# Kernel tuning notes

Hardware: AMD Instinct MI355X
Metric: run time of the kernel (lower is better)

The kernel has to match this reference:

```python
import jax, jax.numpy as jnp
import numpy as np

D_MODEL = 1024
N_HEAD = 16
HEAD_SIZE = D_MODEL // N_HEAD
SEQ = 2048
BATCH = 4
LN_EPS = 1e-5


def layer_norm(x, gamma, beta):
    mu = jnp.mean(x, axis=-1, keepdims=True)
    var = jnp.var(x, axis=-1, keepdims=True)
    return (x - mu) * jax.lax.rsqrt(var + LN_EPS) * gamma + beta


def setup_inputs() -> dict:
    key = jax.random.key(0)
    ks = jax.random.split(key, 12)
    s = 0.02
    return {
        "x": jax.random.normal(ks[0], (BATCH, SEQ, D_MODEL), jnp.float32),
        "Wq": jax.random.normal(ks[1], (N_HEAD, D_MODEL, HEAD_SIZE), jnp.float32) * s,
        "Wk": jax.random.normal(ks[2], (N_HEAD, D_MODEL, HEAD_SIZE), jnp.float32) * s,
        "Wv": jax.random.normal(ks[3], (N_HEAD, D_MODEL, HEAD_SIZE), jnp.float32) * s,
        "Wo": jax.random.normal(ks[4], (D_MODEL, D_MODEL), jnp.float32) * s,
        "bo": jnp.zeros((D_MODEL,), jnp.float32),
        "W1": jax.random.normal(ks[5], (D_MODEL, 4 * D_MODEL), jnp.float32) * s,
        "b1": jnp.zeros((4 * D_MODEL,), jnp.float32),
        "W2": jax.random.normal(ks[6], (4 * D_MODEL, D_MODEL), jnp.float32) * s,
        "b2": jnp.zeros((D_MODEL,), jnp.float32),
        "g1": jnp.ones((D_MODEL,), jnp.float32),
        "be1": jnp.zeros((D_MODEL,), jnp.float32),
        "g2": jnp.ones((D_MODEL,), jnp.float32),
        "be2": jnp.zeros((D_MODEL,), jnp.float32),
    }


def reference(x, Wq, Wk, Wv, Wo, bo, W1, b1, W2, b2, g1, be1, g2, be2):
    B, T, C = x.shape
    # --- self-attention branch (dropout = eval identity) ---
    h = layer_norm(x, g1, be1)
    q = jnp.einsum('btc,hcs->bhts', h, Wq)
    k = jnp.einsum('btc,hcs->bhts', h, Wk)
    v = jnp.einsum('btc,hcs->bhts', h, Wv)
    wei = jnp.einsum('bhts,bhus->bhtu', q, k) * (HEAD_SIZE ** -0.5)
    # non-standard diagonal mask: scores on the diagonal are set to 0 (not -inf)
    diag = jnp.eye(T, dtype=bool)
    wei = jnp.where(diag, jnp.zeros((), wei.dtype), wei)
    wei = jax.nn.softmax(wei, axis=-1)
    att = jnp.einsum('bhtu,bhus->bhts', wei, v)          # [B,H,T,hs]
    att = att.transpose(0, 2, 1, 3).reshape(B, T, C)      # concat heads
    sa = att @ Wo + bo
    x = x + sa
    # --- feed-forward branch ---
    h2 = layer_norm(x, g2, be2)
    ff = jax.nn.gelu(h2 @ W1 + b1, approximate=False) @ W2 + b2
    return x + ff
```

## Files before the change

### kernel.cpp

```cpp
#include <hip/hip_runtime.h>
#include <hip/hip_bf16.h>
#include <math.h>

#define D_MODEL 1024
#define N_HEAD 16
#define HEAD 64
#define SEQ 2048
#define BATCH 4
#define ROWS (BATCH*SEQ)
#define FFD 4096

typedef __bf16 bf16;
typedef __attribute__((ext_vector_type(8))) __bf16 bf16x8;
typedef __attribute__((ext_vector_type(4))) __bf16 bf16x4;
typedef __attribute__((ext_vector_type(4))) float f32x4;
typedef __attribute__((ext_vector_type(4))) short short4v;

static_assert(sizeof(bf16x8) == 16, "bf16x8 must be 16B");

__device__ __forceinline__ void async_copy16(const void* g, void* l) {
  __builtin_amdgcn_global_load_lds((const __attribute__((address_space(1))) void*)g,
                                   (__attribute__((address_space(3))) void*)l, 16, 0, 0);
}

__device__ __forceinline__ bf16x8 dsr16(const bf16* p) {
  bf16x8 r;
  const __attribute__((address_space(3))) bf16* lp =
      (const __attribute__((address_space(3))) bf16*)(unsigned int)(size_t)p;
  asm volatile("ds_read_b128 %0, %1" : "=v"(r) : "v"(lp));
  return r;
}

#define BAR() asm volatile("s_barrier" ::: "memory")

__device__ __forceinline__ f32x4 mfma16(bf16x8 a, bf16x8 b, f32x4 c) {
  return __builtin_amdgcn_mfma_f32_16x16x32_bf16(a, b, c, 0, 0, 0);
}

__device__ __forceinline__ f32x4 mfma16k16(bf16x4 a, bf16x4 b, f32x4 c) {
#if __has_builtin(__builtin_amdgcn_mfma_f32_16x16x16_bf16)
  return __builtin_amdgcn_mfma_f32_16x16x16_bf16(a, b, c, 0, 0, 0);
#else
  return __builtin_amdgcn_mfma_f32_16x16x16bf16_1k(__builtin_bit_cast(short4v, a),
                                                   __builtin_bit_cast(short4v, b), c, 0, 0, 0);
#endif
}

__device__ __forceinline__ float fast_exp2(float x) {
#if __has_builtin(__builtin_amdgcn_exp2f)
  return __builtin_amdgcn_exp2f(x);
#else
  float r; asm("v_exp_f32 %0, %1" : "=v"(r) : "v"(x)); return r;
#endif
}

__device__ __forceinline__ float fast_gelu(float x) {
  const float y = 0.7978845608f * (x + 0.044715f * x * x * x);
  const float e = fast_exp2(y * 2.88539008178f);
  return 0.5f * x * (1.f + (1.f - 2.f / (e + 1.f)));
}

__global__ __launch_bounds__(256) void transpose_cast_kernel(const float* __restrict__ in,
                                                             bf16* __restrict__ out,
                                                             int R, int C) {
  __shared__ float ts[32][33];
  const int r0 = blockIdx.y * 32, c0 = blockIdx.x * 32;
  const int t = threadIdx.x, lr = t >> 3, lc = (t & 7) * 4;
  const float4 v = *(const float4*)(in + (size_t)(r0 + lr) * C + c0 + lc);
  ts[lr][lc + 0] = v.x; ts[lr][lc + 1] = v.y; ts[lr][lc + 2] = v.z; ts[lr][lc + 3] = v.w;
  __syncthreads();
  bf16x4 o;
  o[0] = (bf16)ts[lc + 0][lr]; o[1] = (bf16)ts[lc + 1][lr];
  o[2] = (bf16)ts[lc + 2][lr]; o[3] = (bf16)ts[lc + 3][lr];
  *(bf16x4*)(out + (size_t)(c0 + lr) * R + r0 + lc) = o;
}

__global__ __launch_bounds__(256) void qkv_transpose_kernel(const float* __restrict__ Wq,
                                                            const float* __restrict__ Wk,
                                                            const float* __restrict__ Wv,
                                                            bf16* __restrict__ out) {
  __shared__ float ts[32][33];
  const int mat = blockIdx.z / N_HEAD, h = blockIdx.z % N_HEAD;
  const float* W = (mat == 0 ? Wq : mat == 1 ? Wk : Wv) + (size_t)h * D_MODEL * HEAD;
  bf16* o = out + (size_t)mat * D_MODEL * D_MODEL + (size_t)(h * HEAD) * D_MODEL;
  const int c0 = blockIdx.x * 32, s0 = blockIdx.y * 32;
  const int t = threadIdx.x, lr = t >> 3, lc = (t & 7) * 4;
  const float4 v = *(const float4*)(W + (size_t)(c0 + lr) * HEAD + s0 + lc);
  ts[lr][lc + 0] = v.x; ts[lr][lc + 1] = v.y; ts[lr][lc + 2] = v.z; ts[lr][lc + 3] = v.w;
  __syncthreads();
  bf16x4 ov;
  ov[0] = (bf16)ts[lc + 0][lr]; ov[1] = (bf16)ts[lc + 1][lr];
  ov[2] = (bf16)ts[lc + 2][lr]; ov[3] = (bf16)ts[lc + 3][lr];
  *(bf16x4*)(o + (size_t)(s0 + lr) * D_MODEL + c0 + lc) = ov;
}

__global__ __launch_bounds__(256) void ln_kernel(const float* __restrict__ x,
                                                 const float* __restrict__ g,
                                                 const float* __restrict__ b,
                                                 bf16* __restrict__ h) {
  const int row = blockIdx.x, t = threadIdx.x;
  const float4 v = *(const float4*)(x + (size_t)row * D_MODEL + t * 4);
  float s = v.x + v.y + v.z + v.w;
  float ss = v.x * v.x + v.y * v.y + v.z * v.z + v.w * v.w;
#pragma unroll
  for (int m = 1; m < 64; m <<= 1) { s += __shfl_xor(s, m); ss += __shfl_xor(ss, m); }
  __shared__ float red[8];
  const int wave = t >> 6, lane = t & 63;
  if (lane == 0) { red[wave] = s; red[4 + wave] = ss; }
  __syncthreads();
  s = red[0] + red[1] + red[2] + red[3];
  ss = red[4] + red[5] + red[6] + red[7];
  const float mu = s * (1.f / D_MODEL);
  const float rstd = rsqrtf(ss * (1.f / D_MODEL) - mu * mu + 1e-5f);
  const float4 gv = *(const float4*)(g + t * 4);
  const float4 bv = *(const float4*)(b + t * 4);
  bf16x4 o;
  o[0] = (bf16)((v.x - mu) * rstd * gv.x + bv.x);
  o[1] = (bf16)((v.y - mu) * rstd * gv.y + bv.y);
  o[2] = (bf16)((v.z - mu) * rstd * gv.z + bv.z);
  o[3] = (bf16)((v.w - mu) * rstd * gv.w + bv.w);
  *(bf16x4*)(h + (size_t)row * D_MODEL + t * 4) = o;
}

#define STAGE_A(kt2, h)                                                          \
  do {                                                                           \
    const int off_ = (kt2) * 64 + (h) * 32;                                      \
    bf16* d_ = aDst0 + (((kt2) & 1) * 2 + (h)) * AHALF;                          \
    async_copy16(aSrc0 + off_, d_);                                              \
    if (ASTEPS == 2) async_copy16(aSrc1 + off_, d_ + 4096);                      \
  } while (0)

#define STAGE_B(kt2, h)                                                          \
  do {                                                                           \
    const int off_ = (kt2) * 64 + (h) * 32;                                      \
    bf16* d_ = bDst0 + (((kt2) & 1) * 2 + (h)) * 8192;                           \
    async_copy16(bSrc0 + off_, d_);                                              \
    async_copy16(bSrc1 + off_, d_ + 4096);                                       \
  } while (0)

template <int EPI, int BM>
__device__ __forceinline__ void gemm_body(const bf16* A, const bf16* Bt, int K,
                                          void* outp, const float* bias,
                                          const float* resid, bf16* q_out,
                                          bf16* k_out, bf16* vt_out, int N) {
  constexpr int ASTEPS = BM / 128;
  constexpr int MPW = BM / 2;
  constexpr int MREP = MPW / 16;
  constexpr int MH = MREP / 2;
  constexpr int AHALF = BM * 32;
  __shared__ bf16 As[2 * 2 * BM * 32];
  __shared__ bf16 Bs[2 * 2 * 256 * 32];
  const int t = threadIdx.x, wave = t >> 6, lane = t & 63;
  const int l15 = lane & 15, l4 = lane >> 4;
  const int lin = ((int)blockIdx.x & 7) * ((int)gridDim.x >> 3) + ((int)blockIdx.x >> 3);
  const int nbn = N >> 8;
  const int nbm = (int)gridDim.x / nbn;
  const int bm = lin % nbm, bn = lin / nbm;
  const int nk = K >> 6;

  const int sc = (lane & 3) ^ ((lane >> 3) & 3);
  const int r0 = wave * 16 + (lane >> 2);
  const bf16* aSrc0 = A + (size_t)(bm * BM + r0) * K + sc * 8;
  const bf16* aSrc1 = (ASTEPS == 2) ? (A + (size_t)(bm * BM + 128 + r0) * K + sc * 8) : aSrc0;
  const bf16* bSrc0 = Bt + (size_t)(bn * 256 + r0) * K + sc * 8;
  const bf16* bSrc1 = Bt + (size_t)(bn * 256 + 128 + r0) * K + sc * 8;
  bf16* aDst0 = As + wave * 512;
  bf16* bDst0 = Bs + wave * 512;

  const int wm = wave >> 2, wn = wave & 3;
  const int rw = wm * MPW, cw = wn * 64;
  const int pc = (l4 ^ ((l15 >> 1) & 3)) * 8;

  f32x4 acc[MREP][4];
#pragma unroll
  for (int mi = 0; mi < MREP; mi++)
#pragma unroll
    for (int ni = 0; ni < 4; ni++) { f32x4 z = {0.f, 0.f, 0.f, 0.f}; acc[mi][ni] = z; }

  STAGE_A(0, 0); STAGE_B(0, 0); STAGE_A(0, 1); STAGE_B(0, 1);
  STAGE_B(1, 0); STAGE_A(1, 0); STAGE_B(1, 1);
  if constexpr (ASTEPS == 2) asm volatile("s_waitcnt vmcnt(6)" ::: "memory");
  else                       asm volatile("s_waitcnt vmcnt(5)" ::: "memory");
  BAR();
  __builtin_amdgcn_sched_barrier(0);

  for (int kt = 0; kt < nk; kt++) {
    const bf16* Ab = As + (kt & 1) * (2 * AHALF);
    const bf16* Bb = Bs + (kt & 1) * 16384;
    bf16x8 aF[MH], bF[4];

    if (kt + 1 < nk) STAGE_A(kt + 1, 1);
#pragma unroll
    for (int mi = 0; mi < MH; mi++) aF[mi] = dsr16(Ab + (rw + mi * 16 + l15) * 32 + pc);
#pragma unroll
    for (int ni = 0; ni < 4; ni++) bF[ni] = dsr16(Bb + (cw + ni * 16 + l15) * 32 + pc);
    asm volatile("s_waitcnt lgkmcnt(0)" ::: "memory");
    BAR();
    __builtin_amdgcn_sched_barrier(0);
    __builtin_amdgcn_s_setprio(1);
#pragma unroll
    for (int mi = 0; mi < MH; mi++)
#pragma unroll
      for (int ni = 0; ni < 4; ni++) acc[mi][ni] = mfma16(aF[mi], bF[ni], acc[mi][ni]);
    __builtin_amdgcn_s_setprio(0);

    if (kt + 2 < nk) STAGE_B(kt + 2, 0);
#pragma unroll
    for (int mi = 0; mi < MH; mi++) aF[mi] = dsr16(Ab + (rw + (MH + mi) * 16 + l15) * 32 + pc);
    asm volatile("s_waitcnt lgkmcnt(0)" ::: "memory");
    BAR();
    __builtin_amdgcn_sched_barrier(0);
    __builtin_amdgcn_s_setprio(1);
#pragma unroll
    for (int mi = 0; mi < MH; mi++)
#pragma unroll
      for (int ni = 0; ni < 4; ni++) acc[MH + mi][ni] = mfma16(aF[mi], bF[ni], acc[MH + mi][ni]);
    __builtin_amdgcn_s_setprio(0);

    if (kt + 2 < nk) STAGE_A(kt + 2, 0);
#pragma unroll
    for (int mi = 0; mi < MH; mi++) aF[mi] = dsr16(Ab + AHALF + (rw + mi * 16 + l15) * 32 + pc);
#pragma unroll
    for (int ni = 0; ni < 4; ni++) bF[ni] = dsr16(Bb + 8192 + (cw + ni * 16 + l15) * 32 + pc);
    asm volatile("s_waitcnt lgkmcnt(0)" ::: "memory");
    BAR();
    __builtin_amdgcn_sched_barrier(0);
    __builtin_amdgcn_s_setprio(1);
#pragma unroll
    for (int mi = 0; mi < MH; mi++)
#pragma unroll
      for (int ni = 0; ni < 4; ni++) acc[mi][ni] = mfma16(aF[mi], bF[ni], acc[mi][ni]);
    __builtin_amdgcn_s_setprio(0);

    if (kt + 2 < nk) STAGE_B(kt + 2, 1);
#pragma unroll
    for (int mi = 0; mi < MH; mi++) aF[mi] = dsr16(Ab + AHALF + (rw + (MH + mi) * 16 + l15) * 32 + pc);
    if (kt + 2 < nk) {
      if constexpr (ASTEPS == 2) asm volatile("s_waitcnt vmcnt(6)" ::: "memory");
      else                       asm volatile("s_waitcnt vmcnt(5)" ::: "memory");
    } else {
      asm volatile("s_waitcnt vmcnt(0)" ::: "memory");
    }
    asm volatile("s_waitcnt lgkmcnt(0)" ::: "memory");
    BAR();
    __builtin_amdgcn_sched_barrier(0);
    __builtin_amdgcn_s_setprio(1);
#pragma unroll
    for (int mi = 0; mi < MH; mi++)
#pragma unroll
      for (int ni = 0; ni < 4; ni++) acc[MH + mi][ni] = mfma16(aF[mi], bF[ni], acc[MH + mi][ni]);
    __builtin_amdgcn_s_setprio(0);
  }

#pragma unroll
  for (int mi = 0; mi < MREP; mi++) {
#pragma unroll
    for (int ni = 0; ni < 4; ni++) {
      const int n = bn * 256 + cw + ni * 16 + l15;
#pragma unroll
      for (int e = 0; e < 4; e++) {
        const int m = bm * BM + rw + mi * 16 + l4 * 4 + e;
        float val = acc[mi][ni][e];
        if constexpr (EPI == 0) {
          const int b = m >> 11, tt = m & 2047;
          if (n < D_MODEL) {
            const int hh = n >> 6, sgl = n & 63;
            q_out[(size_t)((b * N_HEAD + hh) * SEQ + tt) * HEAD + sgl] = (bf16)val;
          } else if (n < 2 * D_MODEL) {
            const int n2 = n - D_MODEL, hh = n2 >> 6, sgl = n2 & 63;
            k_out[(size_t)((b * N_HEAD + hh) * SEQ + tt) * HEAD + sgl] = (bf16)val;
          } else {
            const int n2 = n - 2 * D_MODEL, hh = n2 >> 6, sgl = n2 & 63;
            vt_out[(size_t)((b * N_HEAD + hh) * HEAD + sgl) * SEQ + tt] = (bf16)val;
          }
        } else if constexpr (EPI == 1) {
          ((float*)outp)[(size_t)m * N + n] = val + bias[n] + resid[(size_t)m * N + n];
        } else if constexpr (EPI == 2) {
          ((bf16*)outp)[(size_t)m * N + n] = (bf16)fast_gelu(val + bias[n]);
        } else {
          ((float*)outp)[(size_t)m * N + n] = val + bias[n] + resid[(size_t)m * N + n];
        }
      }
    }
  }
}

#undef STAGE_A
#undef STAGE_B

__global__ __launch_bounds__(512, 2) void gemm_qkv_kernel(const bf16* __restrict__ A,
                                                          const bf16* __restrict__ Bt,
                                                          bf16* __restrict__ q_out,
                                                          bf16* __restrict__ k_out,
                                                          bf16* __restrict__ vt_out) {
  gemm_body<0, 256>(A, Bt, D_MODEL, nullptr, nullptr, nullptr, q_out, k_out, vt_out, 3 * D_MODEL);
}

__global__ __launch_bounds__(512, 2) void gemm_proj_kernel(const bf16* __restrict__ A,
                                                           const bf16* __restrict__ Bt,
                                                           float* __restrict__ outp,
                                                           const float* __restrict__ bias,
                                                           const float* __restrict__ resid) {
  gemm_body<1, 128>(A, Bt, D_MODEL, outp, bias, resid, nullptr, nullptr, nullptr, D_MODEL);
}

__global__ __launch_bounds__(512, 2) void gemm_ff1_kernel(const bf16* __restrict__ A,
                                                          const bf16* __restrict__ Bt,
                                                          bf16* __restrict__ outp,
                                                          const float* __restrict__ bias) {
  gemm_body<2, 256>(A, Bt, D_MODEL, outp, bias, nullptr, nullptr, nullptr, nullptr, FFD);
}

__global__ __launch_bounds__(512, 2) void gemm_ff2_kernel(const bf16* __restrict__ A,
                                                          const bf16* __restrict__ Bt,
                                                          float* __restrict__ outp,
                                                          const float* __restrict__ bias,
                                                          const float* __restrict__ resid) {
  gemm_body<3, 128>(A, Bt, FFD, outp, bias, resid, nullptr, nullptr, nullptr, D_MODEL);
}

__global__ __launch_bounds__(256, 2) void attn_kernel(const bf16* __restrict__ q,
                                                      const bf16* __restrict__ k,
                                                      const bf16* __restrict__ vt,
                                                      bf16* __restrict__ att) {
  __shared__ bf16 Ks[64 * 64];
  __shared__ bf16 Vs[64 * 64];
  const int t = threadIdx.x, wave = t >> 6, lane = t & 63;
  const int l15 = lane & 15, l4 = lane >> 4;
  const int bh = blockIdx.x & 63, qblk = blockIdx.x >> 6;
  const bf16* qb = q + (size_t)bh * SEQ * HEAD;
  const bf16* kb = k + (size_t)bh * SEQ * HEAD;
  const bf16* vb = vt + (size_t)bh * HEAD * SEQ;
  const int qrow = qblk * 256 + wave * 64;

  const int tr = t >> 3, tc = t & 7, sw = tc ^ (tr & 7);
  const bf16* ksrc0 = kb + (size_t)tr * HEAD + sw * 8;
  const bf16* ksrc1 = kb + (size_t)(tr + 32) * HEAD + sw * 8;
  const bf16* vsrc0 = vb + (size_t)tr * SEQ + sw * 8;
  const bf16* vsrc1 = vb + (size_t)(tr + 32) * SEQ + sw * 8;
  bf16* kd0 = Ks + t * 8; bf16* kd1 = Ks + t * 8 + 2048;
  bf16* vd0 = Vs + t * 8; bf16* vd1 = Vs + t * 8 + 2048;

  const float qscale = 0.125f * 1.44269504088896340736f;
  bf16x8 qf[4][2];
#pragma unroll
  for (int qs = 0; qs < 4; qs++)
#pragma unroll
    for (int h = 0; h < 2; h++) {
      const bf16x8 raw = *(const bf16x8*)(qb + (size_t)(qrow + qs * 16 + l15) * HEAD + h * 32 + l4 * 8);
      bf16x8 sc;
#pragma unroll
      for (int e = 0; e < 8; e++) sc[e] = (bf16)((float)raw[e] * qscale);
      qf[qs][h] = sc;
    }

  f32x4 o[4][4];
  float lsum[4] = {0.f, 0.f, 0.f, 0.f};
#pragma unroll
  for (int qs = 0; qs < 4; qs++)
#pragma unroll
    for (int dm = 0; dm < 4; dm++) { f32x4 z = {0.f, 0.f, 0.f, 0.f}; o[qs][dm] = z; }

  const int rsw = l15 & 7;

  for (int u0 = 0; u0 < SEQ; u0 += 64) {
    __syncthreads();
    async_copy16(ksrc0 + (size_t)u0 * HEAD, kd0);
    async_copy16(ksrc1 + (size_t)u0 * HEAD, kd1);
    async_copy16(vsrc0 + u0, vd0);
    async_copy16(vsrc1 + u0, vd1);
    __syncthreads();

    bf16x8 kf[4][2];
#pragma unroll
    for (int n = 0; n < 4; n++)
#pragma unroll
      for (int h = 0; h < 2; h++)
        kf[n][h] = *(const bf16x8*)(Ks + (n * 16 + l15) * 64 + (((h << 2) | l4) ^ rsw) * 8);
    bf16x4 vf[4][4];
#pragma unroll
    for (int dm = 0; dm < 4; dm++)
#pragma unroll
      for (int n = 0; n < 4; n++)
        vf[dm][n] = *(const bf16x4*)(Vs + (dm * 16 + l15) * 64 + ((((n << 1) | (l4 >> 1)) ^ rsw) * 8) + (l4 & 1) * 4);

#pragma unroll
    for (int qs = 0; qs < 4; qs++) {
      f32x4 s[4];
#pragma unroll
      for (int n = 0; n < 4; n++) {
        f32x4 c = {0.f, 0.f, 0.f, 0.f};
        c = mfma16(kf[n][0], qf[qs][0], c);
        c = mfma16(kf[n][1], qf[qs][1], c);
        s[n] = c;
      }
      if (u0 == qrow) {
#pragma unroll
        for (int r = 0; r < 4; r++)
          s[qs][r] = (l15 == l4 * 4 + r) ? 0.f : s[qs][r];
      }
      bf16x4 pf[4];
      float ls = 0.f;
#pragma unroll
      for (int n = 0; n < 4; n++) {
        f32x4 pv;
#pragma unroll
        for (int r = 0; r < 4; r++) { pv[r] = fast_exp2(s[n][r]); ls += pv[r]; }
        bf16x4 pb;
#pragma unroll
        for (int r = 0; r < 4; r++) pb[r] = (bf16)pv[r];
        pf[n] = pb;
      }
      lsum[qs] += ls;
#pragma unroll
      for (int dm = 0; dm < 4; dm++) {
        f32x4 acc = o[qs][dm];
#pragma unroll
        for (int n = 0; n < 4; n++) acc = mfma16k16(vf[dm][n], pf[n], acc);
        o[qs][dm] = acc;
      }
    }
  }

#pragma unroll
  for (int qs = 0; qs < 4; qs++) {
    float l = lsum[qs];
    l += __shfl_xor(l, 16);
    l += __shfl_xor(l, 32);
    lsum[qs] = l;
  }
  const int b = bh >> 4, hh = bh & 15;
#pragma unroll
  for (int qs = 0; qs < 4; qs++) {
    const float linv = 1.0f / lsum[qs];
#pragma unroll
    for (int dm = 0; dm < 4; dm++) {
      bf16x4 ov;
#pragma unroll
      for (int r = 0; r < 4; r++) ov[r] = (bf16)(o[qs][dm][r] * linv);
      *(bf16x4*)(att + (size_t)(b * SEQ + qrow + qs * 16 + l15) * D_MODEL + hh * HEAD + dm * 16 + l4 * 4) = ov;
    }
  }
}

extern "C" void kernel_launch(void* const* d_in, const int* in_sizes, int n_in,
                              void* d_out, int out_size, void* d_ws, size_t ws_size,
                              hipStream_t stream) {
  const float* x   = (const float*)d_in[0];
  const float* Wq  = (const float*)d_in[1];
  const float* Wk  = (const float*)d_in[2];
  const float* Wv  = (const float*)d_in[3];
  const float* Wo  = (const float*)d_in[4];
  const float* bo  = (const float*)d_in[5];
  const float* W1  = (const float*)d_in[6];
  const float* b1  = (const float*)d_in[7];
  const float* W2  = (const float*)d_in[8];
  const float* b2  = (const float*)d_in[9];
  const float* g1  = (const float*)d_in[10];
  const float* be1 = (const float*)d_in[11];
  const float* g2  = (const float*)d_in[12];
  const float* be2 = (const float*)d_in[13];
  float* out = (float*)d_out;

  bf16* Wqkv_t = (bf16*)d_ws;
  bf16* Wo_t   = Wqkv_t + (size_t)3 * D_MODEL * D_MODEL;
  bf16* W1_t   = Wo_t + (size_t)D_MODEL * D_MODEL;
  bf16* W2_t   = W1_t + (size_t)FFD * D_MODEL;
  bf16* hbuf   = W2_t + (size_t)D_MODEL * FFD;
  float* x1    = (float*)(hbuf + (size_t)ROWS * D_MODEL);
  bf16* big    = (bf16*)(x1 + (size_t)ROWS * D_MODEL);
  bf16* qbuf   = big;
  bf16* kbuf   = qbuf + (size_t)ROWS * D_MODEL;
  bf16* vtbuf  = kbuf + (size_t)ROWS * D_MODEL;
  bf16* ffbuf  = big;
  bf16* attb   = big + (size_t)ROWS * FFD;

  qkv_transpose_kernel<<<dim3(D_MODEL / 32, HEAD / 32, 3 * N_HEAD), 256, 0, stream>>>(Wq, Wk, Wv, Wqkv_t);
  transpose_cast_kernel<<<dim3(D_MODEL / 32, D_MODEL / 32), 256, 0, stream>>>(Wo, Wo_t, D_MODEL, D_MODEL);
  transpose_cast_kernel<<<dim3(FFD / 32, D_MODEL / 32), 256, 0, stream>>>(W1, W1_t, D_MODEL, FFD);
  transpose_cast_kernel<<<dim3(D_MODEL / 32, FFD / 32), 256, 0, stream>>>(W2, W2_t, FFD, D_MODEL);
  ln_kernel<<<ROWS, 256, 0, stream>>>(x, g1, be1, hbuf);
  gemm_qkv_kernel<<<dim3((3 * D_MODEL / 256) * (ROWS / 256)), 512, 0, stream>>>(
      hbuf, Wqkv_t, qbuf, kbuf, vtbuf);
  attn_kernel<<<64 * (SEQ / 256), 256, 0, stream>>>(qbuf, kbuf, vtbuf, attb);
  gemm_proj_kernel<<<dim3((D_MODEL / 256) * (ROWS / 128)), 512, 0, stream>>>(
      attb, Wo_t, x1, bo, x);
  ln_kernel<<<ROWS, 256, 0, stream>>>(x1, g2, be2, hbuf);
  gemm_ff1_kernel<<<dim3((FFD / 256) * (ROWS / 256)), 512, 0, stream>>>(
      hbuf, W1_t, ffbuf, b1);
  gemm_ff2_kernel<<<dim3((D_MODEL / 256) * (ROWS / 128)), 512, 0, stream>>>(
      ffbuf, W2_t, out, b2, x1);
}
```

Before: 572.9 us.

## Switch GEMMs to 128x128 tiles with 4 waves and triple-buffered K=32 pipeline

Replaces the 8-wave 256-wide GEMM tiles, which used double-buffered 64-wide K steps split into four sub-phases, with 4-wave 128x128 tiles. These use a three-slot ring of 32-wide K stages, prefetch two stages ahead, and hit one barrier per stage. The aim is a simpler pipeline, higher occupancy (3 blocks per CU) and more blocks for better load balance. The trade-offs are less data reuse per tile, more global and L2 traffic, and a barrier for every 32 elements of K.

```diff
diff --git a/kernel.cpp b/kernel.cpp
--- a/kernel.cpp
+++ b/kernel.cpp
@@ -122,144 +122,89 @@
   *(bf16x4*)(h + (size_t)row * D_MODEL + t * 4) = o;
 }
 
-#define STAGE_A(kt2, h)                                                          \
+#define STG(soff, rg)                                                            \
   do {                                                                           \
-    const int off_ = (kt2) * 64 + (h) * 32;                                      \
-    bf16* d_ = aDst0 + (((kt2) & 1) * 2 + (h)) * AHALF;                          \
-    async_copy16(aSrc0 + off_, d_);                                              \
-    if (ASTEPS == 2) async_copy16(aSrc1 + off_, d_ + 4096);                      \
+    const int o_ = (soff) * 32;                                                  \
+    bf16* ad_ = aDst + (rg) * 4096;                                              \
+    bf16* bd_ = bDst + (rg) * 4096;                                              \
+    async_copy16(aSrc0 + o_, ad_);                                               \
+    async_copy16(aSrc1 + o_, ad_ + 2048);                                        \
+    async_copy16(bSrc0 + o_, bd_);                                               \
+    async_copy16(bSrc1 + o_, bd_ + 2048);                                        \
   } while (0)
 
-#define STAGE_B(kt2, h)                                                          \
-  do {                                                                           \
-    const int off_ = (kt2) * 64 + (h) * 32;                                      \
-    bf16* d_ = bDst0 + (((kt2) & 1) * 2 + (h)) * 8192;                           \
-    async_copy16(bSrc0 + off_, d_);                                              \
-    async_copy16(bSrc1 + off_, d_ + 4096);                                       \
-  } while (0)
-
-template <int EPI, int BM>
+template <int EPI>
 __device__ __forceinline__ void gemm_body(const bf16* A, const bf16* Bt, int K,
                                           void* outp, const float* bias,
                                           const float* resid, bf16* q_out,
                                           bf16* k_out, bf16* vt_out, int N) {
-  constexpr int ASTEPS = BM / 128;
-  constexpr int MPW = BM / 2;
-  constexpr int MREP = MPW / 16;
-  constexpr int MH = MREP / 2;
-  constexpr int AHALF = BM * 32;
-  __shared__ bf16 As[2 * 2 * BM * 32];
-  __shared__ bf16 Bs[2 * 2 * 256 * 32];
+  __shared__ __align__(16) bf16 As[3 * 128 * 32];
+  __shared__ __align__(16) bf16 Bs[3 * 128 * 32];
   const int t = threadIdx.x, wave = t >> 6, lane = t & 63;
   const int l15 = lane & 15, l4 = lane >> 4;
   const int lin = ((int)blockIdx.x & 7) * ((int)gridDim.x >> 3) + ((int)blockIdx.x >> 3);
-  const int nbn = N >> 8;
+  const int nbn = N >> 7;
   const int nbm = (int)gridDim.x / nbn;
   const int bm = lin % nbm, bn = lin / nbm;
-  const int nk = K >> 6;
+  const int ns = K >> 5;
 
   const int sc = (lane & 3) ^ ((lane >> 3) & 3);
   const int r0 = wave * 16 + (lane >> 2);
-  const bf16* aSrc0 = A + (size_t)(bm * BM + r0) * K + sc * 8;
-  const bf16* aSrc1 = (ASTEPS == 2) ? (A + (size_t)(bm * BM + 128 + r0) * K + sc * 8) : aSrc0;
-  const bf16* bSrc0 = Bt + (size_t)(bn * 256 + r0) * K + sc * 8;
-  const bf16* bSrc1 = Bt + (size_t)(bn * 256 + 128 + r0) * K + sc * 8;
-  bf16* aDst0 = As + wave * 512;
-  bf16* bDst0 = Bs + wave * 512;
-
-  const int wm = wave >> 2, wn = wave & 3;
-  const int rw = wm * MPW, cw = wn * 64;
+  const bf16* aSrc0 = A + (size_t)(bm * 128 + r0) * K + sc * 8;
+  const bf16* aSrc1 = A + (size_t)(bm * 128 + 64 + r0) * K + sc * 8;
+  const bf16* bSrc0 = Bt + (size_t)(bn * 128 + r0) * K + sc * 8;
+  const bf16* bSrc1 = Bt + (size_t)(bn * 128 + 64 + r0) * K + sc * 8;
+  bf16* aDst = As + wave * 512;
+  bf16* bDst = Bs + wave * 512;
+
+  const int rw = (wave >> 1) * 64, cw = (wave & 1) * 64;
   const int pc = (l4 ^ ((l15 >> 1) & 3)) * 8;
 
-  f32x4 acc[MREP][4];
-#pragma unroll
-  for (int mi = 0; mi < MREP; mi++)
+  f32x4 acc[4][4];
+#pragma unroll
+  for (int mi = 0; mi < 4; mi++)
 #pragma unroll
     for (int ni = 0; ni < 4; ni++) { f32x4 z = {0.f, 0.f, 0.f, 0.f}; acc[mi][ni] = z; }
 
-  STAGE_A(0, 0); STAGE_B(0, 0); STAGE_A(0, 1); STAGE_B(0, 1);
-  STAGE_B(1, 0); STAGE_A(1, 0); STAGE_B(1, 1);
-  if constexpr (ASTEPS == 2) asm volatile("s_waitcnt vmcnt(6)" ::: "memory");
-  else                       asm volatile("s_waitcnt vmcnt(5)" ::: "memory");
+  STG(0, 0);
+  STG(1, 1);
+  asm volatile("s_waitcnt vmcnt(4)" ::: "memory");
   BAR();
   __builtin_amdgcn_sched_barrier(0);
 
-  for (int kt = 0; kt < nk; kt++) {
-    const bf16* Ab = As + (kt & 1) * (2 * AHALF);
-    const bf16* Bb = Bs + (kt & 1) * 16384;
-    bf16x8 aF[MH], bF[4];
-
-    if (kt + 1 < nk) STAGE_A(kt + 1, 1);
-#pragma unroll
-    for (int mi = 0; mi < MH; mi++) aF[mi] = dsr16(Ab + (rw + mi * 16 + l15) * 32 + pc);
+  int reg = 0, sreg = 2;
+  for (int s = 0; s < ns; ++s) {
+    const bf16* Ab = As + reg * 4096;
+    const bf16* Bb = Bs + reg * 4096;
+    if (s + 2 < ns) STG(s + 2, sreg);
+    bf16x8 aF[4], bF[4];
+#pragma unroll
+    for (int mi = 0; mi < 4; mi++) aF[mi] = dsr16(Ab + (rw + mi * 16 + l15) * 32 + pc);
 #pragma unroll
     for (int ni = 0; ni < 4; ni++) bF[ni] = dsr16(Bb + (cw + ni * 16 + l15) * 32 + pc);
+    if (s + 2 < ns) asm volatile("s_waitcnt vmcnt(4)" ::: "memory");
+    else            asm volatile("s_waitcnt vmcnt(0)" ::: "memory");
     asm volatile("s_waitcnt lgkmcnt(0)" ::: "memory");
     BAR();
     __builtin_amdgcn_sched_barrier(0);
     __builtin_amdgcn_s_setprio(1);
 #pragma unroll
-    for (int mi = 0; mi < MH; mi++)
+    for (int mi = 0; mi < 4; mi++)
 #pragma unroll
       for (int ni = 0; ni < 4; ni++) acc[mi][ni] = mfma16(aF[mi], bF[ni], acc[mi][ni]);
     __builtin_amdgcn_s_setprio(0);
-
-    if (kt + 2 < nk) STAGE_B(kt + 2, 0);
-#pragma unroll
-    for (int mi = 0; mi < MH; mi++) aF[mi] = dsr16(Ab + (rw + (MH + mi) * 16 + l15) * 32 + pc);
-    asm volatile("s_waitcnt lgkmcnt(0)" ::: "memory");
-    BAR();
-    __builtin_amdgcn_sched_barrier(0);
-    __builtin_amdgcn_s_setprio(1);
-#pragma unroll
-    for (int mi = 0; mi < MH; mi++)
-#pragma unroll
-      for (int ni = 0; ni < 4; ni++) acc[MH + mi][ni] = mfma16(aF[mi], bF[ni], acc[MH + mi][ni]);
-    __builtin_amdgcn_s_setprio(0);
-
-    if (kt + 2 < nk) STAGE_A(kt + 2, 0);
-#pragma unroll
-    for (int mi = 0; mi < MH; mi++) aF[mi] = dsr16(Ab + AHALF + (rw + mi * 16 + l15) * 32 + pc);
-#pragma unroll
-    for (int ni = 0; ni < 4; ni++) bF[ni] = dsr16(Bb + 8192 + (cw + ni * 16 + l15) * 32 + pc);
-    asm volatile("s_waitcnt lgkmcnt(0)" ::: "memory");
-    BAR();
-    __builtin_amdgcn_sched_barrier(0);
-    __builtin_amdgcn_s_setprio(1);
-#pragma unroll
-    for (int mi = 0; mi < MH; mi++)
-#pragma unroll
-      for (int ni = 0; ni < 4; ni++) acc[mi][ni] = mfma16(aF[mi], bF[ni], acc[mi][ni]);
-    __builtin_amdgcn_s_setprio(0);
-
-    if (kt + 2 < nk) STAGE_B(kt + 2, 1);
-#pragma unroll
-    for (int mi = 0; mi < MH; mi++) aF[mi] = dsr16(Ab + AHALF + (rw + (MH + mi) * 16 + l15) * 32 + pc);
-    if (kt + 2 < nk) {
-      if constexpr (ASTEPS == 2) asm volatile("s_waitcnt vmcnt(6)" ::: "memory");
-      else                       asm volatile("s_waitcnt vmcnt(5)" ::: "memory");
-    } else {
-      asm volatile("s_waitcnt vmcnt(0)" ::: "memory");
-    }
-    asm volatile("s_waitcnt lgkmcnt(0)" ::: "memory");
-    BAR();
-    __builtin_amdgcn_sched_barrier(0);
-    __builtin_amdgcn_s_setprio(1);
-#pragma unroll
-    for (int mi = 0; mi < MH; mi++)
-#pragma unroll
-      for (int ni = 0; ni < 4; ni++) acc[MH + mi][ni] = mfma16(aF[mi], bF[ni], acc[MH + mi][ni]);
-    __builtin_amdgcn_s_setprio(0);
+    reg = (reg == 2) ? 0 : reg + 1;
+    sreg = (sreg == 2) ? 0 : sreg + 1;
   }
 
 #pragma unroll
-  for (int mi = 0; mi < MREP; mi++) {
+  for (int mi = 0; mi < 4; mi++) {
 #pragma unroll
     for (int ni = 0; ni < 4; ni++) {
-      const int n = bn * 256 + cw + ni * 16 + l15;
+      const int n = bn * 128 + cw + ni * 16 + l15;
 #pragma unroll
       for (int e = 0; e < 4; e++) {
-        const int m = bm * BM + rw + mi * 16 + l4 * 4 + e;
+        const int m = bm * 128 + rw + mi * 16 + l4 * 4 + e;
         float val = acc[mi][ni][e];
         if constexpr (EPI == 0) {
           const int b = m >> 11, tt = m & 2047;
@@ -285,38 +230,37 @@
   }
 }
 
-#undef STAGE_A
-#undef STAGE_B
-
-__global__ __launch_bounds__(512, 2) void gemm_qkv_kernel(const bf16* __restrict__ A,
+#undef STG
+
+__global__ __launch_bounds__(256, 3) void gemm_qkv_kernel(const bf16* __restrict__ A,
                                                           const bf16* __restrict__ Bt,
                                                           bf16* __restrict__ q_out,
                                                           bf16* __restrict__ k_out,
                                                           bf16* __restrict__ vt_out) {
-  gemm_body<0, 256>(A, Bt, D_MODEL, nullptr, nullptr, nullptr, q_out, k_out, vt_out, 3 * D_MODEL);
-}
-
-__global__ __launch_bounds__(512, 2) void gemm_proj_kernel(const bf16* __restrict__ A,
+  gemm_body<0>(A, Bt, D_MODEL, nullptr, nullptr, nullptr, q_out, k_out, vt_out, 3 * D_MODEL);
+}
+
+__global__ __launch_bounds__(256, 3) void gemm_proj_kernel(const bf16* __restrict__ A,
                                                            const bf16* __restrict__ Bt,
                                                            float* __restrict__ outp,
                                                            const float* __restrict__ bias,
                                                            const float* __restrict__ resid) {
-  gemm_body<1, 128>(A, Bt, D_MODEL, outp, bias, resid, nullptr, nullptr, nullptr, D_MODEL);
-}
-
-__global__ __launch_bounds__(512, 2) void gemm_ff1_kernel(const bf16* __restrict__ A,
+  gemm_body<1>(A, Bt, D_MODEL, outp, bias, resid, nullptr, nullptr, nullptr, D_MODEL);
+}
+
+__global__ __launch_bounds__(256, 3) void gemm_ff1_kernel(const bf16* __restrict__ A,
                                                           const bf16* __restrict__ Bt,
                                                           bf16* __restrict__ outp,
                                                           const float* __restrict__ bias) {
-  gemm_body<2, 256>(A, Bt, D_MODEL, outp, bias, nullptr, nullptr, nullptr, nullptr, FFD);
-}
-
-__global__ __launch_bounds__(512, 2) void gemm_ff2_kernel(const bf16* __restrict__ A,
+  gemm_body<2>(A, Bt, D_MODEL, outp, bias, nullptr, nullptr, nullptr, nullptr, FFD);
+}
+
+__global__ __launch_bounds__(256, 3) void gemm_ff2_kernel(const bf16* __restrict__ A,
                                                           const bf16* __restrict__ Bt,
                                                           float* __restrict__ outp,
                                                           const float* __restrict__ bias,
                                                           const float* __restrict__ resid) {
-  gemm_body<3, 128>(A, Bt, FFD, outp, bias, resid, nullptr, nullptr, nullptr, D_MODEL);
+  gemm_body<3>(A, Bt, FFD, outp, bias, resid, nullptr, nullptr, nullptr, D_MODEL);
 }
 
 __global__ __launch_bounds__(256, 2) void attn_kernel(const bf16* __restrict__ q,
@@ -480,14 +424,14 @@
   transpose_cast_kernel<<<dim3(FFD / 32, D_MODEL / 32), 256, 0, stream>>>(W1, W1_t, D_MODEL, FFD);
   transpose_cast_kernel<<<dim3(D_MODEL / 32, FFD / 32), 256, 0, stream>>>(W2, W2_t, FFD, D_MODEL);
   ln_kernel<<<ROWS, 256, 0, stream>>>(x, g1, be1, hbuf);
-  gemm_qkv_kernel<<<dim3((3 * D_MODEL / 256) * (ROWS / 256)), 512, 0, stream>>>(
+  gemm_qkv_kernel<<<dim3((3 * D_MODEL / 128) * (ROWS / 128)), 256, 0, stream>>>(
       hbuf, Wqkv_t, qbuf, kbuf, vtbuf);
   attn_kernel<<<64 * (SEQ / 256), 256, 0, stream>>>(qbuf, kbuf, vtbuf, attb);
-  gemm_proj_kernel<<<dim3((D_MODEL / 256) * (ROWS / 128)), 512, 0, stream>>>(
+  gemm_proj_kernel<<<dim3((D_MODEL / 128) * (ROWS / 128)), 256, 0, stream>>>(
       attb, Wo_t, x1, bo, x);
   ln_kernel<<<ROWS, 256, 0, stream>>>(x1, g2, be2, hbuf);
-  gemm_ff1_kernel<<<dim3((FFD / 256) * (ROWS / 256)), 512, 0, stream>>>(
+  gemm_ff1_kernel<<<dim3((FFD / 128) * (ROWS / 128)), 256, 0, stream>>>(
       hbuf, W1_t, ffbuf, b1);
-  gemm_ff2_kernel<<<dim3((D_MODEL / 256) * (ROWS / 128)), 512, 0, stream>>>(
+  gemm_ff2_kernel<<<dim3((D_MODEL / 128) * (ROWS / 128)), 256, 0, stream>>>(
       ffbuf, W2_t, out, b2, x1);
 }
```

Result: faster. 559.9 us (-2.3%).

## Restructure GEMM pipeline into separate 256/128 bodies with one-stage prefetch

Applied to the files above, without the earlier changes.

Splits the templated GEMM into dedicated 256-row and 128-row bodies with a simpler double-buffered schedule: fragments are read before issuing the next tile's async copies, with extra barriers between sub-steps. The QKV GEMM moves to 128-row tiles (doubling its grid), and the block index mapping changes to iterate N-tiles fastest. The goal is to cut register pressure and improve occupancy and L2 reuse, but it adds barriers and shortens the prefetch distance from two sub-stages to one, which may expose more memory latency.

```diff
diff --git a/kernel.cpp b/kernel.cpp
--- a/kernel.cpp
+++ b/kernel.cpp
@@ -32,6 +32,8 @@
 }
 
 #define BAR() asm volatile("s_barrier" ::: "memory")
+#define LGKM0() do { asm volatile("s_waitcnt lgkmcnt(0)" ::: "memory"); \
+                     __builtin_amdgcn_sched_barrier(0); } while (0)
 
 __device__ __forceinline__ f32x4 mfma16(bf16x8 a, bf16x8 b, f32x4 c) {
   return __builtin_amdgcn_mfma_f32_16x16x32_bf16(a, b, c, 0, 0, 0);
@@ -122,178 +124,246 @@
   *(bf16x4*)(h + (size_t)row * D_MODEL + t * 4) = o;
 }
 
-#define STAGE_A(kt2, h)                                                          \
-  do {                                                                           \
-    const int off_ = (kt2) * 64 + (h) * 32;                                      \
-    bf16* d_ = aDst0 + (((kt2) & 1) * 2 + (h)) * AHALF;                          \
-    async_copy16(aSrc0 + off_, d_);                                              \
-    if (ASTEPS == 2) async_copy16(aSrc1 + off_, d_ + 4096);                      \
-  } while (0)
-
-#define STAGE_B(kt2, h)                                                          \
-  do {                                                                           \
-    const int off_ = (kt2) * 64 + (h) * 32;                                      \
-    bf16* d_ = bDst0 + (((kt2) & 1) * 2 + (h)) * 8192;                           \
-    async_copy16(bSrc0 + off_, d_);                                              \
-    async_copy16(bSrc1 + off_, d_ + 4096);                                       \
-  } while (0)
-
-template <int EPI, int BM>
-__device__ __forceinline__ void gemm_body(const bf16* A, const bf16* Bt, int K,
-                                          void* outp, const float* bias,
-                                          const float* resid, bf16* q_out,
-                                          bf16* k_out, bf16* vt_out, int N) {
-  constexpr int ASTEPS = BM / 128;
-  constexpr int MPW = BM / 2;
-  constexpr int MREP = MPW / 16;
-  constexpr int MH = MREP / 2;
-  constexpr int AHALF = BM * 32;
-  __shared__ bf16 As[2 * 2 * BM * 32];
-  __shared__ bf16 Bs[2 * 2 * 256 * 32];
+template <int EPI>
+__device__ __forceinline__ void gemm_epi(int m, int n, float val, void* outp,
+                                         const float* bias, const float* resid,
+                                         bf16* q_out, bf16* k_out, bf16* vt_out, int N) {
+  if constexpr (EPI == 0) {
+    const int b = m >> 11, tt = m & 2047;
+    if (n < D_MODEL) {
+      const int hh = n >> 6, sgl = n & 63;
+      q_out[(size_t)((b * N_HEAD + hh) * SEQ + tt) * HEAD + sgl] = (bf16)val;
+    } else if (n < 2 * D_MODEL) {
+      const int n2 = n - D_MODEL, hh = n2 >> 6, sgl = n2 & 63;
+      k_out[(size_t)((b * N_HEAD + hh) * SEQ + tt) * HEAD + sgl] = (bf16)val;
+    } else {
+      const int n2 = n - 2 * D_MODEL, hh = n2 >> 6, sgl = n2 & 63;
+      vt_out[(size_t)((b * N_HEAD + hh) * HEAD + sgl) * SEQ + tt] = (bf16)val;
+    }
+  } else if constexpr (EPI == 1) {
+    ((float*)outp)[(size_t)m * N + n] = val + bias[n] + resid[(size_t)m * N + n];
+  } else if constexpr (EPI == 2) {
+    ((bf16*)outp)[(size_t)m * N + n] = (bf16)fast_gelu(val + bias[n]);
+  } else {
+    ((float*)outp)[(size_t)m * N + n] = val + bias[n] + resid[(size_t)m * N + n];
+  }
+}
+
+template <int EPI>
+__device__ __forceinline__ void gemm_body256(const bf16* A, const bf16* Bt, int K,
+                                             void* outp, const float* bias,
+                                             const float* resid, bf16* q_out,
+                                             bf16* k_out, bf16* vt_out, int N) {
+  __shared__ __align__(16) bf16 As[2 * 2 * 8192];
+  __shared__ __align__(16) bf16 Bs[2 * 2 * 8192];
   const int t = threadIdx.x, wave = t >> 6, lane = t & 63;
   const int l15 = lane & 15, l4 = lane >> 4;
   const int lin = ((int)blockIdx.x & 7) * ((int)gridDim.x >> 3) + ((int)blockIdx.x >> 3);
   const int nbn = N >> 8;
-  const int nbm = (int)gridDim.x / nbn;
-  const int bm = lin % nbm, bn = lin / nbm;
+  const int bn = lin % nbn, bm = lin / nbn;
   const int nk = K >> 6;
 
   const int sc = (lane & 3) ^ ((lane >> 3) & 3);
   const int r0 = wave * 16 + (lane >> 2);
-  const bf16* aSrc0 = A + (size_t)(bm * BM + r0) * K + sc * 8;
-  const bf16* aSrc1 = (ASTEPS == 2) ? (A + (size_t)(bm * BM + 128 + r0) * K + sc * 8) : aSrc0;
+  const bf16* aSrc0 = A + (size_t)(bm * 256 + r0) * K + sc * 8;
+  const bf16* aSrc1 = A + (size_t)(bm * 256 + 128 + r0) * K + sc * 8;
   const bf16* bSrc0 = Bt + (size_t)(bn * 256 + r0) * K + sc * 8;
   const bf16* bSrc1 = Bt + (size_t)(bn * 256 + 128 + r0) * K + sc * 8;
-  bf16* aDst0 = As + wave * 512;
-  bf16* bDst0 = Bs + wave * 512;
 
   const int wm = wave >> 2, wn = wave & 3;
-  const int rw = wm * MPW, cw = wn * 64;
+  const int rw = wm * 128, cw = wn * 64;
   const int pc = (l4 ^ ((l15 >> 1) & 3)) * 8;
 
-  f32x4 acc[MREP][4];
-#pragma unroll
-  for (int mi = 0; mi < MREP; mi++)
+#define STG_A(kt2, kk)                                                              \
+  do { const int o_ = (kt2) * 64 + (kk) * 32;                                       \
+       bf16* d_ = As + (((kt2) & 1) * 2 + (kk)) * 8192 + wave * 512;                \
+       async_copy16(aSrc0 + o_, d_); async_copy16(aSrc1 + o_, d_ + 4096); } while (0)
+#define STG_B(kt2, kk)                                                              \
+  do { const int o_ = (kt2) * 64 + (kk) * 32;                                       \
+       bf16* d_ = Bs + (((kt2) & 1) * 2 + (kk)) * 8192 + wave * 512;                \
+       async_copy16(bSrc0 + o_, d_); async_copy16(bSrc1 + o_, d_ + 4096); } while (0)
+
+  f32x4 acc[8][4];
+#pragma unroll
+  for (int mi = 0; mi < 8; mi++)
 #pragma unroll
     for (int ni = 0; ni < 4; ni++) { f32x4 z = {0.f, 0.f, 0.f, 0.f}; acc[mi][ni] = z; }
 
-  STAGE_A(0, 0); STAGE_B(0, 0); STAGE_A(0, 1); STAGE_B(0, 1);
-  STAGE_B(1, 0); STAGE_A(1, 0); STAGE_B(1, 1);
-  if constexpr (ASTEPS == 2) asm volatile("s_waitcnt vmcnt(6)" ::: "memory");
-  else                       asm volatile("s_waitcnt vmcnt(5)" ::: "memory");
+  STG_A(0, 0); STG_B(0, 0); STG_A(0, 1); STG_B(0, 1);
+  asm volatile("s_waitcnt vmcnt(4)" ::: "memory");
   BAR();
   __builtin_amdgcn_sched_barrier(0);
 
   for (int kt = 0; kt < nk; kt++) {
-    const bf16* Ab = As + (kt & 1) * (2 * AHALF);
+    const bf16* Ab = As + (kt & 1) * 16384;
     const bf16* Bb = Bs + (kt & 1) * 16384;
-    bf16x8 aF[MH], bF[4];
-
-    if (kt + 1 < nk) STAGE_A(kt + 1, 1);
-#pragma unroll
-    for (int mi = 0; mi < MH; mi++) aF[mi] = dsr16(Ab + (rw + mi * 16 + l15) * 32 + pc);
+    const bool pf = (kt + 1 < nk);
+    bf16x8 aF[4], bF[4];
+
+#pragma unroll
+    for (int mi = 0; mi < 4; mi++) aF[mi] = dsr16(Ab + (rw + mi * 16 + l15) * 32 + pc);
 #pragma unroll
     for (int ni = 0; ni < 4; ni++) bF[ni] = dsr16(Bb + (cw + ni * 16 + l15) * 32 + pc);
-    asm volatile("s_waitcnt lgkmcnt(0)" ::: "memory");
-    BAR();
-    __builtin_amdgcn_sched_barrier(0);
+    if (pf) STG_A(kt + 1, 0);
+    BAR();
+    LGKM0();
     __builtin_amdgcn_s_setprio(1);
 #pragma unroll
-    for (int mi = 0; mi < MH; mi++)
+    for (int mi = 0; mi < 4; mi++)
 #pragma unroll
       for (int ni = 0; ni < 4; ni++) acc[mi][ni] = mfma16(aF[mi], bF[ni], acc[mi][ni]);
     __builtin_amdgcn_s_setprio(0);
-
-    if (kt + 2 < nk) STAGE_B(kt + 2, 0);
-#pragma unroll
-    for (int mi = 0; mi < MH; mi++) aF[mi] = dsr16(Ab + (rw + (MH + mi) * 16 + l15) * 32 + pc);
-    asm volatile("s_waitcnt lgkmcnt(0)" ::: "memory");
-    BAR();
-    __builtin_amdgcn_sched_barrier(0);
+    BAR();
+
+#pragma unroll
+    for (int mi = 0; mi < 4; mi++) aF[mi] = dsr16(Ab + (rw + (4 + mi) * 16 + l15) * 32 + pc);
+    if (pf) STG_B(kt + 1, 0);
+    BAR();
+    LGKM0();
     __builtin_amdgcn_s_setprio(1);
 #pragma unroll
-    for (int mi = 0; mi < MH; mi++)
-#pragma unroll
-      for (int ni = 0; ni < 4; ni++) acc[MH + mi][ni] = mfma16(aF[mi], bF[ni], acc[MH + mi][ni]);
+    for (int mi = 0; mi < 4; mi++)
+#pragma unroll
+      for (int ni = 0; ni < 4; ni++) acc[4 + mi][ni] = mfma16(aF[mi], bF[ni], acc[4 + mi][ni]);
     __builtin_amdgcn_s_setprio(0);
-
-    if (kt + 2 < nk) STAGE_A(kt + 2, 0);
-#pragma unroll
-    for (int mi = 0; mi < MH; mi++) aF[mi] = dsr16(Ab + AHALF + (rw + mi * 16 + l15) * 32 + pc);
+    if (pf) asm volatile("s_waitcnt vmcnt(4)" ::: "memory");
+    else    asm volatile("s_waitcnt vmcnt(0)" ::: "memory");
+    BAR();
+
+#pragma unroll
+    for (int mi = 0; mi < 4; mi++) aF[mi] = dsr16(Ab + 8192 + (rw + mi * 16 + l15) * 32 + pc);
 #pragma unroll
     for (int ni = 0; ni < 4; ni++) bF[ni] = dsr16(Bb + 8192 + (cw + ni * 16 + l15) * 32 + pc);
-    asm volatile("s_waitcnt lgkmcnt(0)" ::: "memory");
-    BAR();
-    __builtin_amdgcn_sched_barrier(0);
+    if (pf) STG_A(kt + 1, 1);
+    BAR();
+    LGKM0();
     __builtin_amdgcn_s_setprio(1);
 #pragma unroll
-    for (int mi = 0; mi < MH; mi++)
+    for (int mi = 0; mi < 4; mi++)
 #pragma unroll
       for (int ni = 0; ni < 4; ni++) acc[mi][ni] = mfma16(aF[mi], bF[ni], acc[mi][ni]);
     __builtin_amdgcn_s_setprio(0);
-
-    if (kt + 2 < nk) STAGE_B(kt + 2, 1);
-#pragma unroll
-    for (int mi = 0; mi < MH; mi++) aF[mi] = dsr16(Ab + AHALF + (rw + (MH + mi) * 16 + l15) * 32 + pc);
-    if (kt + 2 < nk) {
-      if constexpr (ASTEPS == 2) asm volatile("s_waitcnt vmcnt(6)" ::: "memory");
-      else                       asm volatile("s_waitcnt vmcnt(5)" ::: "memory");
-    } else {
-      asm volatile("s_waitcnt vmcnt(0)" ::: "memory");
-    }
-    asm volatile("s_waitcnt lgkmcnt(0)" ::: "memory");
-    BAR();
-    __builtin_amdgcn_sched_barrier(0);
+    BAR();
+
+#pragma unroll
+    for (int mi = 0; mi < 4; mi++) aF[mi] = dsr16(Ab + 8192 + (rw + (4 + mi) * 16 + l15) * 32 + pc);
+    if (pf) STG_B(kt + 1, 1);
+    BAR();
+    LGKM0();
     __builtin_amdgcn_s_setprio(1);
 #pragma unroll
-    for (int mi = 0; mi < MH; mi++)
-#pragma unroll
-      for (int ni = 0; ni < 4; ni++) acc[MH + mi][ni] = mfma16(aF[mi], bF[ni], acc[MH + mi][ni]);
+    for (int mi = 0; mi < 4; mi++)
+#pragma unroll
+      for (int ni = 0; ni < 4; ni++) acc[4 + mi][ni] = mfma16(aF[mi], bF[ni], acc[4 + mi][ni]);
     __builtin_amdgcn_s_setprio(0);
+    if (pf) asm volatile("s_waitcnt vmcnt(4)" ::: "memory");
+    else    asm volatile("s_waitcnt vmcnt(0)" ::: "memory");
+    BAR();
   }
-
-#pragma unroll
-  for (int mi = 0; mi < MREP; mi++) {
+#undef STG_A
+#undef STG_B
+
+#pragma unroll
+  for (int mi = 0; mi < 8; mi++)
 #pragma unroll
     for (int ni = 0; ni < 4; ni++) {
       const int n = bn * 256 + cw + ni * 16 + l15;
 #pragma unroll
       for (int e = 0; e < 4; e++) {
-        const int m = bm * BM + rw + mi * 16 + l4 * 4 + e;
-        float val = acc[mi][ni][e];
-        if constexpr (EPI == 0) {
-          const int b = m >> 11, tt = m & 2047;
-          if (n < D_MODEL) {
-            const int hh = n >> 6, sgl = n & 63;
-            q_out[(size_t)((b * N_HEAD + hh) * SEQ + tt) * HEAD + sgl] = (bf16)val;
-          } else if (n < 2 * D_MODEL) {
-            const int n2 = n - D_MODEL, hh = n2 >> 6, sgl = n2 & 63;
-            k_out[(size_t)((b * N_HEAD + hh) * SEQ + tt) * HEAD + sgl] = (bf16)val;
-          } else {
-            const int n2 = n - 2 * D_MODEL, hh = n2 >> 6, sgl = n2 & 63;
-            vt_out[(size_t)((b * N_HEAD + hh) * HEAD + sgl) * SEQ + tt] = (bf16)val;
-          }
-        } else if constexpr (EPI == 1) {
-          ((float*)outp)[(size_t)m * N + n] = val + bias[n] + resid[(size_t)m * N + n];
-        } else if constexpr (EPI == 2) {
-          ((bf16*)outp)[(size_t)m * N + n] = (bf16)fast_gelu(val + bias[n]);
-        } else {
-          ((float*)outp)[(size_t)m * N + n] = val + bias[n] + resid[(size_t)m * N + n];
-        }
+        const int m = bm * 256 + rw + mi * 16 + l4 * 4 + e;
+        gemm_epi<EPI>(m, n, acc[mi][ni][e], outp, bias, resid, q_out, k_out, vt_out, N);
       }
     }
+}
+
+template <int EPI>
+__device__ __forceinline__ void gemm_body128(const bf16* A, const bf16* Bt, int K,
+                                             void* outp, const float* bias,
+                                             const float* resid, bf16* q_out,
+                                             bf16* k_out, bf16* vt_out, int N) {
+  __shared__ __align__(16) bf16 As[2 * 2 * 4096];
+  __shared__ __align__(16) bf16 Bs[2 * 2 * 8192];
+  const int t = threadIdx.x, wave = t >> 6, lane = t & 63;
+  const int l15 = lane & 15, l4 = lane >> 4;
+  const int lin = ((int)blockIdx.x & 7) * ((int)gridDim.x >> 3) + ((int)blockIdx.x >> 3);
+  const int nbn = N >> 8;
+  const int bn = lin % nbn, bm = lin / nbn;
+  const int nk = K >> 6;
+
+  const int sc = (lane & 3) ^ ((lane >> 3) & 3);
+  const int r0 = wave * 16 + (lane >> 2);
+  const bf16* aSrc0 = A + (size_t)(bm * 128 + r0) * K + sc * 8;
+  const bf16* bSrc0 = Bt + (size_t)(bn * 256 + r0) * K + sc * 8;
+  const bf16* bSrc1 = Bt + (size_t)(bn * 256 + 128 + r0) * K + sc * 8;
+
+  const int wm = wave >> 2, wn = wave & 3;
+  const int rw = wm * 64, cw = wn * 64;
+  const int pc = (l4 ^ ((l15 >> 1) & 3)) * 8;
+
+#define STG(kt2, kk)                                                                \
+  do { const int o_ = (kt2) * 64 + (kk) * 32;                                       \
+       bf16* ad_ = As + (((kt2) & 1) * 2 + (kk)) * 4096 + wave * 512;               \
+       bf16* bd_ = Bs + (((kt2) & 1) * 2 + (kk)) * 8192 + wave * 512;               \
+       async_copy16(aSrc0 + o_, ad_);                                               \
+       async_copy16(bSrc0 + o_, bd_); async_copy16(bSrc1 + o_, bd_ + 4096); } while (0)
+
+  f32x4 acc[4][4];
+#pragma unroll
+  for (int mi = 0; mi < 4; mi++)
+#pragma unroll
+    for (int ni = 0; ni < 4; ni++) { f32x4 z = {0.f, 0.f, 0.f, 0.f}; acc[mi][ni] = z; }
+
+  STG(0, 0); STG(0, 1);
+  asm volatile("s_waitcnt vmcnt(3)" ::: "memory");
+  BAR();
+  __builtin_amdgcn_sched_barrier(0);
+
+  for (int kt = 0; kt < nk; kt++) {
+    const bool pf = (kt + 1 < nk);
+    bf16x8 aF[4], bF[4];
+#pragma unroll
+    for (int kk = 0; kk < 2; kk++) {
+      const bf16* Ab = As + ((kt & 1) * 2 + kk) * 4096;
+      const bf16* Bb = Bs + ((kt & 1) * 2 + kk) * 8192;
+#pragma unroll
+      for (int mi = 0; mi < 4; mi++) aF[mi] = dsr16(Ab + (rw + mi * 16 + l15) * 32 + pc);
+#pragma unroll
+      for (int ni = 0; ni < 4; ni++) bF[ni] = dsr16(Bb + (cw + ni * 16 + l15) * 32 + pc);
+      if (pf) STG(kt + 1, kk);
+      BAR();
+      LGKM0();
+      __builtin_amdgcn_s_setprio(1);
+#pragma unroll
+      for (int mi = 0; mi < 4; mi++)
+#pragma unroll
+        for (int ni = 0; ni < 4; ni++) acc[mi][ni] = mfma16(aF[mi], bF[ni], acc[mi][ni]);
+      __builtin_amdgcn_s_setprio(0);
+      if (pf) asm volatile("s_waitcnt vmcnt(3)" ::: "memory");
+      else    asm volatile("s_waitcnt vmcnt(0)" ::: "memory");
+      BAR();
+    }
   }
-}
-
-#undef STAGE_A
-#undef STAGE_B
+#undef STG
+
+#pragma unroll
+  for (int mi = 0; mi < 4; mi++)
+#pragma unroll
+    for (int ni = 0; ni < 4; ni++) {
+      const int n = bn * 256 + cw + ni * 16 + l15;
+#pragma unroll
+      for (int e = 0; e < 4; e++) {
+        const int m = bm * 128 + rw + mi * 16 + l4 * 4 + e;
+        gemm_epi<EPI>(m, n, acc[mi][ni][e], outp, bias, resid, q_out, k_out, vt_out, N);
+      }
+    }
+}
 
 __global__ __launch_bounds__(512, 2) void gemm_qkv_kernel(const bf16* __restrict__ A,
                                                           const bf16* __restrict__ Bt,
                                                           bf16* __restrict__ q_out,
                                                           bf16* __restrict__ k_out,
                                                           bf16* __restrict__ vt_out) {
-  gemm_body<0, 256>(A, Bt, D_MODEL, nullptr, nullptr, nullptr, q_out, k_out, vt_out, 3 * D_MODEL);
+  gemm_body128<0>(A, Bt, D_MODEL, nullptr, nullptr, nullptr, q_out, k_out, vt_out, 3 * D_MODEL);
 }
 
 __global__ __launch_bounds__(512, 2) void gemm_proj_kernel(const bf16* __restrict__ A,
@@ -301,14 +371,14 @@
                                                            float* __restrict__ outp,
                                                            const float* __restrict__ bias,
                                                            const float* __restrict__ resid) {
-  gemm_body<1, 128>(A, Bt, D_MODEL, outp, bias, resid, nullptr, nullptr, nullptr, D_MODEL);
+  gemm_body128<1>(A, Bt, D_MODEL, outp, bias, resid, nullptr, nullptr, nullptr, D_MODEL);
 }
 
 __global__ __launch_bounds__(512, 2) void gemm_ff1_kernel(const bf16* __restrict__ A,
                                                           const bf16* __restrict__ Bt,
                                                           bf16* __restrict__ outp,
                                                           const float* __restrict__ bias) {
-  gemm_body<2, 256>(A, Bt, D_MODEL, outp, bias, nullptr, nullptr, nullptr, nullptr, FFD);
+  gemm_body256<2>(A, Bt, D_MODEL, outp, bias, nullptr, nullptr, nullptr, nullptr, FFD);
 }
 
 __global__ __launch_bounds__(512, 2) void gemm_ff2_kernel(const bf16* __restrict__ A,
@@ -316,7 +386,7 @@
                                                           float* __restrict__ outp,
                                                           const float* __restrict__ bias,
                                                           const float* __restrict__ resid) {
-  gemm_body<3, 128>(A, Bt, FFD, outp, bias, resid, nullptr, nullptr, nullptr, D_MODEL);
+  gemm_body128<3>(A, Bt, FFD, outp, bias, resid, nullptr, nullptr, nullptr, D_MODEL);
 }
 
 __global__ __launch_bounds__(256, 2) void attn_kernel(const bf16* __restrict__ q,
@@ -480,7 +550,7 @@
   transpose_cast_kernel<<<dim3(FFD / 32, D_MODEL / 32), 256, 0, stream>>>(W1, W1_t, D_MODEL, FFD);
   transpose_cast_kernel<<<dim3(D_MODEL / 32, FFD / 32), 256, 0, stream>>>(W2, W2_t, FFD, D_MODEL);
   ln_kernel<<<ROWS, 256, 0, stream>>>(x, g1, be1, hbuf);
-  gemm_qkv_kernel<<<dim3((3 * D_MODEL / 256) * (ROWS / 256)), 512, 0, stream>>>(
+  gemm_qkv_kernel<<<dim3((3 * D_MODEL / 256) * (ROWS / 128)), 512, 0, stream>>>(
       hbuf, Wqkv_t, qbuf, kbuf, vtbuf);
   attn_kernel<<<64 * (SEQ / 256), 256, 0, stream>>>(qbuf, kbuf, vtbuf, attb);
   gemm_proj_kernel<<<dim3((D_MODEL / 256) * (ROWS / 128)), 512, 0, stream>>>(
```

Result: faster. 524.5 us (-8.5%).
